# Optimization experiments

Measured on AMD Instinct MI355X. Metric: run time of the kernel, lower is better.

## Reference

```python
import jax, jax.numpy as jnp
import numpy as np

NUM_EMBEDDINGS = 8192
EMBED_DIM = 256
BETA = 0.25  # commitment loss weight (self.beta in the torch module)


def setup_inputs() -> dict:
    key = jax.random.key(0)
    k1, k2 = jax.random.split(key)
    z = jax.random.normal(k1, (16, EMBED_DIM, 32, 32), dtype=jnp.float32)
    # learned codebook (nn.Embedding weight), default init ~ N(0,1); scale for realism
    codebook = jax.random.normal(k2, (NUM_EMBEDDINGS, EMBED_DIM), dtype=jnp.float32)
    return {"z": z, "codebook": codebook}


def reference(z, codebook):
    # channel_last: [B, C, H, W] -> [B, H, W, C]
    zl = jnp.transpose(z, (0, 2, 3, 1))
    # d = ||e||^2 - 2 z.e  (the ||z||^2 term is constant w.r.t. argmin, as in source)
    d = jnp.sum(codebook * codebook, axis=1) - 2.0 * jnp.einsum('bhwd,nd->bhwn', zl, codebook)
    index = jnp.argmin(d, axis=-1)          # [B, H, W] int
    z_q = codebook[index]                   # [B, H, W, C]
    loss = (jnp.mean((jax.lax.stop_gradient(z_q) - zl) ** 2)
            + BETA * jnp.mean((z_q - jax.lax.stop_gradient(zl)) ** 2))
    # straight-through estimator
    z_q_st = zl + jax.lax.stop_gradient(z_q - zl)
    # diversity: mean over batch of (#unique codes used per sample) / (#positions per sample)
    B = index.shape[0]
    flat = index.reshape(B, -1)             # [B, HW]
    presence = jnp.zeros((B, NUM_EMBEDDINGS), jnp.float32).at[
        jnp.arange(B)[:, None], flat].set(1.0)
    diversity = presence.sum() / jnp.float32(flat.size)
    # channel_first: [B, H, W, C] -> [B, C, H, W]
    z_q_out = jnp.transpose(z_q_st, (0, 3, 1, 2))
    return z_q_out, index, loss, diversity
```

## Files before the change

### kernel.cpp

```cpp
#include <hip/hip_runtime.h>
#include <cstdint>

typedef unsigned short u16;
typedef unsigned int   u32;
typedef __attribute__((ext_vector_type(8))) short bf16x8;
typedef __attribute__((ext_vector_type(4))) float f32x4;

#define NPOS    16384
#define DIM     256
#define NCODES  8192
#define ZSTRIDE 262144
#define NELEM   4194304
#define TAU     6e-3f
#define RCH     32


#define WS_AHI    0u
#define WS_ALO    8388608u
#define WS_BHI    16777216u
#define WS_BLO    20971520u
#define WS_E2     25165824u
#define WS_WV1    25198592u
#define WS_WI1    25722880u
#define WS_WV2    26247168u
#define WS_IDX    26771456u
#define WS_PRES   26836992u
#define WS_RCNT   26853376u
#define WS_LDEL   26853380u
#define WS_RLIST  26853632u
#define WS_PART   26919168u
#define WS_RBV    26920448u
#define WS_RBI    29017600u

__device__ __forceinline__ u16 f2bf(float x) {
    u32 u = __float_as_uint(x);
    return (u16)((u + 0x7FFFu + ((u >> 16) & 1u)) >> 16);
}
__device__ __forceinline__ float bf2f(u16 h) { return __uint_as_float((u32)h << 16); }

__device__ __forceinline__ void gload_lds16(const void* g, void* l) {
    __builtin_amdgcn_global_load_lds(
        (const __attribute__((address_space(1))) void*)g,
        (__attribute__((address_space(3))) void*)l, 16, 0, 0);
}

__device__ __forceinline__ void top2_push(float& v1, int& i1, float& v2, float d, int c) {
    const bool better = d < v1;
    v2 = fminf(v2, fmaxf(d, v1));
    v1 = fminf(v1, d);
    if (better) i1 = c;
}
__device__ __forceinline__ void top2_merge(float& v1, int& i1, float& v2,
                                           float ov1, int oi1, float ov2) {
    const bool better = ov1 < v1;
    v2 = fminf(fminf(v2, ov2), fmaxf(v1, ov1));
    v1 = fminf(v1, ov1);
    if (better) i1 = oi1;
}

__global__ __launch_bounds__(256)
void preprocess(const float* __restrict__ cb, const float* __restrict__ z,
                u16* __restrict__ Bhi, u16* __restrict__ Blo,
                u16* __restrict__ Ahi, u16* __restrict__ Alo,
                float* __restrict__ e2, u32* __restrict__ presence,
                int* __restrict__ rcnt, float* __restrict__ ldel) {
    __shared__ u16 his[128 * 34], los[128 * 34];
    const int bid = blockIdx.x;
    const int t   = threadIdx.x;

    if (bid < 2048) {
        if (bid < 16) presence[bid * 256 + t] = 0u;
        if (bid == 16 && t == 0) { rcnt[0] = 0; ldel[0] = 0.0f; }

        const int row  = bid * 4 + (t >> 6);
        const int lane = t & 63;
        const float4 v = *(const float4*)(cb + (size_t)row * DIM + lane * 4);
        float s = v.x * v.x + v.y * v.y + v.z * v.z + v.w * v.w;
#pragma unroll
        for (int o = 32; o > 0; o >>= 1) s += __shfl_xor(s, o);
        if (lane == 0) e2[row] = s;

        const float vv[4] = {v.x, v.y, v.z, v.w};
        u16 h[4], l[4];
#pragma unroll
        for (int j = 0; j < 4; ++j) { h[j] = f2bf(vv[j]); l[j] = f2bf(vv[j] - bf2f(h[j])); }

        const int nt = row >> 7, pr = row & 127, kt = lane >> 3;
        const int q  = (lane & 7) >> 1, off = (lane & 1) * 4;
        const int sw = (pr >> 1) & 3;
        const size_t dst = ((size_t)(nt * 8 + kt) * 128 + pr) * 32 + ((q ^ sw) << 3) + off;
        *(uint2*)(Bhi + dst) = make_uint2((u32)h[0] | ((u32)h[1] << 16), (u32)h[2] | ((u32)h[3] << 16));
        *(uint2*)(Blo + dst) = make_uint2((u32)l[0] | ((u32)l[1] << 16), (u32)l[2] | ((u32)l[3] << 16));
        return;
    }

    const int zb = bid - 2048;
    const int m = zb >> 3, kt = zb & 7;
    const int b = m >> 3, hw0 = (m & 7) * 128;
    const int p = t & 127, ch = t >> 7;

#pragma unroll
    for (int sub = 0; sub < 16; ++sub) {
        const int cl = sub * 2 + ch;
        const float v = z[(size_t)b * ZSTRIDE + (size_t)(kt * 32 + cl) * 1024 + hw0 + p];
        const u16 h = f2bf(v);
        his[p * 34 + cl] = h;
        los[p * 34 + cl] = f2bf(v - bf2f(h));
    }
    __syncthreads();
    const int p2 = t >> 1, c0 = (t & 1) * 2;
    const int sw = (p2 >> 1) & 3;
    const size_t base = ((size_t)(m * 8 + kt) * 128 + p2) * 32;
    u32 wh[8], wl[8];
    const int half = c0 * 8;
#pragma unroll
    for (int j = 0; j < 8; ++j) {
        wh[j] = (u32)his[p2 * 34 + half + 2 * j] | ((u32)his[p2 * 34 + half + 2 * j + 1] << 16);
        wl[j] = (u32)los[p2 * 34 + half + 2 * j] | ((u32)los[p2 * 34 + half + 2 * j + 1] << 16);
    }
    *(uint4*)(Ahi + base + (((c0 + 0) ^ sw) << 3)) = make_uint4(wh[0], wh[1], wh[2], wh[3]);
    *(uint4*)(Ahi + base + (((c0 + 1) ^ sw) << 3)) = make_uint4(wh[4], wh[5], wh[6], wh[7]);
    *(uint4*)(Alo + base + (((c0 + 0) ^ sw) << 3)) = make_uint4(wl[0], wl[1], wl[2], wl[3]);
    *(uint4*)(Alo + base + (((c0 + 1) ^ sw) << 3)) = make_uint4(wl[4], wl[5], wl[6], wl[7]);
}

__global__ __launch_bounds__(256, 2)
void gemm_argmin(const u16* __restrict__ Ahi, const u16* __restrict__ Alo,
                 const u16* __restrict__ Bhi, const u16* __restrict__ Blo,
                 const float* __restrict__ e2,
                 float* __restrict__ wv1, int* __restrict__ wi1, float* __restrict__ wv2) {
    __shared__ u16 sbuf[2][4][4096];
    __shared__ float lv1[256]; __shared__ int li1[256]; __shared__ float lv2[256];

    const int bid = blockIdx.x;
    const int ng  = bid & 7;
    const int mt  = bid >> 3;

    const int tid  = threadIdx.x;
    const int lane = tid & 63;
    const int wvi  = tid >> 6;
    const int wr   = wvi >> 1, wc = wvi & 1;
    const int l15  = lane & 15, lq = lane >> 4;
    const int woff = (tid & 192) * 16;
    const int src  = tid * 8;
    const int sel  = (l15 >> 1) & 3;
    const int ka   = ((lq ^ sel) << 3);

#define FRAG(base, row) (*(const bf16x8*)((base) + (row) * 32 + ka))
#define STAGE(bq, ss_) do {                                                     \
        const int nt_ = ng * 8 + ((ss_) >> 3), kt_ = (ss_) & 7;                 \
        const u16* Ah_ = Ahi + (size_t)(mt * 8 + kt_) * 4096;                   \
        const u16* Al_ = Alo + (size_t)(mt * 8 + kt_) * 4096;                   \
        const u16* Bh_ = Bhi + (size_t)(nt_ * 8 + kt_) * 4096;                  \
        const u16* Bl_ = Blo + (size_t)(nt_ * 8 + kt_) * 4096;                  \
        gload_lds16(Ah_ + src,        (char*)&sbuf[bq][0][0] + woff);           \
        gload_lds16(Ah_ + 2048 + src, (char*)&sbuf[bq][0][0] + 4096 + woff);    \
        gload_lds16(Al_ + src,        (char*)&sbuf[bq][1][0] + woff);           \
        gload_lds16(Al_ + 2048 + src, (char*)&sbuf[bq][1][0] + 4096 + woff);    \
        gload_lds16(Bh_ + src,        (char*)&sbuf[bq][2][0] + woff);           \
        gload_lds16(Bh_ + 2048 + src, (char*)&sbuf[bq][2][0] + 4096 + woff);    \
        gload_lds16(Bl_ + src,        (char*)&sbuf[bq][3][0] + woff);           \
        gload_lds16(Bl_ + 2048 + src, (char*)&sbuf[bq][3][0] + 4096 + woff);    \
    } while (0)

    float rv1[16], rv2[16]; int ri1[16];
#pragma unroll
    for (int e = 0; e < 16; ++e) { rv1[e] = 3e38f; rv2[e] = 3e38f; ri1[e] = 0; }

    f32x4 acc[4][4] = {};
    float e2v[4];
    int cbase = 0;

    STAGE(0, 0);
    __syncthreads();

    for (int ss = 0; ss < 64; ++ss) {
        const int cur = ss & 1;
        if (ss < 63) STAGE(cur ^ 1, ss + 1);

        if ((ss & 7) == 0) {
            const int nt = ng * 8 + (ss >> 3);
            cbase = nt * 128 + wc * 64 + l15;
#pragma unroll
            for (int ni = 0; ni < 4; ++ni) e2v[ni] = e2[cbase + ni * 16];
        }

        const u16* Ah = &sbuf[cur][0][0];
        const u16* Al = &sbuf[cur][1][0];
        const u16* Bh = &sbuf[cur][2][0];
        const u16* Bl = &sbuf[cur][3][0];

        bf16x8 ah[4], bh[4], xx[4];
#pragma unroll
        for (int i = 0; i < 4; ++i) ah[i] = FRAG(Ah, wr * 64 + i * 16 + l15);
#pragma unroll
        for (int i = 0; i < 4; ++i) bh[i] = FRAG(Bh, wc * 64 + i * 16 + l15);
#pragma unroll
        for (int i = 0; i < 4; ++i)
#pragma unroll
            for (int j = 0; j < 4; ++j)
                acc[i][j] = __builtin_amdgcn_mfma_f32_16x16x32_bf16(ah[i], bh[j], acc[i][j], 0, 0, 0);
#pragma unroll
        for (int i = 0; i < 4; ++i) xx[i] = FRAG(Bl, wc * 64 + i * 16 + l15);
#pragma unroll
        for (int i = 0; i < 4; ++i)
#pragma unroll
            for (int j = 0; j < 4; ++j)
                acc[i][j] = __builtin_amdgcn_mfma_f32_16x16x32_bf16(ah[i], xx[j], acc[i][j], 0, 0, 0);
#pragma unroll
        for (int i = 0; i < 4; ++i) xx[i] = FRAG(Al, wr * 64 + i * 16 + l15);
#pragma unroll
        for (int i = 0; i < 4; ++i)
#pragma unroll
            for (int j = 0; j < 4; ++j)
                acc[i][j] = __builtin_amdgcn_mfma_f32_16x16x32_bf16(xx[i], bh[j], acc[i][j], 0, 0, 0);

        if ((ss & 7) == 7) {
#pragma unroll
            for (int mi = 0; mi < 4; ++mi)
#pragma unroll
                for (int j = 0; j < 4; ++j) {
                    const int e = mi * 4 + j;
#pragma unroll
                    for (int ni = 0; ni < 4; ++ni) {
                        const float d = fmaf(-2.0f, acc[mi][ni][j], e2v[ni]);
                        top2_push(rv1[e], ri1[e], rv2[e], d, cbase + ni * 16);
                    }
                }
#pragma unroll
            for (int mi = 0; mi < 4; ++mi)
#pragma unroll
                for (int ni = 0; ni < 4; ++ni)
                    acc[mi][ni] = f32x4{0.f, 0.f, 0.f, 0.f};
        }
        __syncthreads();
    }

#pragma unroll
    for (int mi = 0; mi < 4; ++mi)
#pragma unroll
        for (int j = 0; j < 4; ++j) {
            const int e = mi * 4 + j;
            float v1 = rv1[e], v2 = rv2[e]; int i1 = ri1[e];
#pragma unroll
            for (int off = 1; off <= 8; off <<= 1) {
                const float ov1 = __shfl_xor(v1, off);
                const int   oi1 = __shfl_xor(i1, off);
                const float ov2 = __shfl_xor(v2, off);
                top2_merge(v1, i1, v2, ov1, oi1, ov2);
            }
            if (l15 == 0) {
                const int row = wr * 64 + mi * 16 + lq * 4 + j;
                lv1[row * 2 + wc] = v1; li1[row * 2 + wc] = i1; lv2[row * 2 + wc] = v2;
            }
        }
    __syncthreads();
    if (tid < 128) {
        float v1 = lv1[tid * 2], v2 = lv2[tid * 2]; int i1 = li1[tid * 2];
        top2_merge(v1, i1, v2, lv1[tid * 2 + 1], li1[tid * 2 + 1], lv2[tid * 2 + 1]);
        const size_t o = (size_t)ng * NPOS + (size_t)mt * 128 + tid;
        wv1[o] = v1; wi1[o] = i1; wv2[o] = v2;
    }
#undef FRAG
#undef STAGE
}

__global__ __launch_bounds__(256)
void merge_output(const float* __restrict__ wv1, const int* __restrict__ wi1,
                  const float* __restrict__ wv2,
                  const float* __restrict__ z, const float* __restrict__ cb,
                  float* __restrict__ out, float* __restrict__ out_idxf,
                  float* __restrict__ partial, u32* __restrict__ presence,
                  int* __restrict__ rcnt, int* __restrict__ rlist,
                  int* __restrict__ ws_idx) {
    __shared__ int codes[64];
    __shared__ float red[256];
    const int tile = blockIdx.x;
    const int b    = tile >> 4;
    const int hw0  = (tile & 15) * 64;
    const int tid  = threadIdx.x;
    const int m    = tid & 63;
    const int cg   = tid >> 6;

    if (cg == 0) {
        const int pos = tile * 64 + m;
        float v1 = 3e38f, v2 = 3e38f; int i1 = 0;
#pragma unroll
        for (int g = 0; g < 8; ++g) {
            const size_t o = (size_t)g * NPOS + pos;
            top2_merge(v1, i1, v2, wv1[o], wi1[o], wv2[o]);
        }
        codes[m]      = i1;
        ws_idx[pos]   = i1;
        out_idxf[pos] = (float)i1;
        if (v2 - v1 < TAU) {
            const int s = atomicAdd(rcnt, 1);
            rlist[s] = pos;
        } else {
            atomicOr(&presence[b * 256 + (i1 >> 5)], 1u << (i1 & 31));
        }
    }
    __syncthreads();

    const int code = codes[m];
    const float* crow = cb  + (size_t)code * DIM;
    const float* zb   = z   + (size_t)b * ZSTRIDE + hw0 + m;
    float*       ob   = out + (size_t)b * ZSTRIDE + hw0 + m;

    float lsum = 0.0f;
#pragma unroll
    for (int q = 0; q < 16; ++q) {
        const int c = (cg * 16 + q) * 4;
        const float4 e = *(const float4*)(crow + c);
        const float z0 = zb[(size_t)(c + 0) * 1024];
        const float z1 = zb[(size_t)(c + 1) * 1024];
        const float z2 = zb[(size_t)(c + 2) * 1024];
        const float z3 = zb[(size_t)(c + 3) * 1024];
        const float d0 = e.x - z0, d1 = e.y - z1, d2 = e.z - z2, d3 = e.w - z3;
        lsum += d0 * d0 + d1 * d1 + d2 * d2 + d3 * d3;
        ob[(size_t)(c + 0) * 1024] = z0 + d0;
        ob[(size_t)(c + 1) * 1024] = z1 + d1;
        ob[(size_t)(c + 2) * 1024] = z2 + d2;
        ob[(size_t)(c + 3) * 1024] = z3 + d3;
    }
    red[tid] = lsum;
    __syncthreads();
    for (int o = 128; o > 0; o >>= 1) {
        if (tid < o) red[tid] += red[tid + o];
        __syncthreads();
    }
    if (tid == 0) partial[tile] = red[0];
}

__global__ __launch_bounds__(256)
void rescue_scan(const float* __restrict__ z, const float* __restrict__ cb,
                 const float* __restrict__ e2, const int* __restrict__ rcnt,
                 const int* __restrict__ rlist,
                 float* __restrict__ rbv, int* __restrict__ rbi) {
    __shared__ float zvec[256];
    __shared__ float sv[256]; __shared__ int si[256];
    const int n = rcnt[0];
    const int t = threadIdx.x;
    for (int idx = blockIdx.x; idx < n * RCH; idx += gridDim.x) {
        const int e  = idx >> 5;
        const int ch = idx & 31;
        const int pos = rlist[e];
        const int b = pos >> 10, hw = pos & 1023;
        __syncthreads();
        zvec[t] = z[(size_t)b * ZSTRIDE + (size_t)t * 1024 + hw];
        __syncthreads();

        const int c = ch * 256 + t;
        const float* cr = cb + (size_t)c * DIM;
        float a0 = 0.f, a1 = 0.f, a2 = 0.f, a3 = 0.f;
#pragma unroll
        for (int k = 0; k < DIM; k += 16) {
            const float4 v0 = *(const float4*)(cr + k);
            const float4 v1 = *(const float4*)(cr + k + 4);
            const float4 v2 = *(const float4*)(cr + k + 8);
            const float4 v3 = *(const float4*)(cr + k + 12);
            a0 = fmaf(zvec[k + 0], v0.x, a0); a0 = fmaf(zvec[k + 1], v0.y, a0);
            a0 = fmaf(zvec[k + 2], v0.z, a0); a0 = fmaf(zvec[k + 3], v0.w, a0);
            a1 = fmaf(zvec[k + 4], v1.x, a1); a1 = fmaf(zvec[k + 5], v1.y, a1);
            a1 = fmaf(zvec[k + 6], v1.z, a1); a1 = fmaf(zvec[k + 7], v1.w, a1);
            a2 = fmaf(zvec[k + 8], v2.x, a2); a2 = fmaf(zvec[k + 9], v2.y, a2);
            a2 = fmaf(zvec[k +10], v2.z, a2); a2 = fmaf(zvec[k +11], v2.w, a2);
            a3 = fmaf(zvec[k +12], v3.x, a3); a3 = fmaf(zvec[k +13], v3.y, a3);
            a3 = fmaf(zvec[k +14], v3.z, a3); a3 = fmaf(zvec[k +15], v3.w, a3);
        }
        const float dot = (a0 + a1) + (a2 + a3);
        sv[t] = fmaf(-2.f, dot, e2[c]); si[t] = c;
        __syncthreads();
        for (int o = 128; o > 0; o >>= 1) {
            if (t < o) {
                const float ov = sv[t + o]; const int oi = si[t + o];
                if (ov < sv[t] || (ov == sv[t] && oi < si[t])) { sv[t] = ov; si[t] = oi; }
            }
            __syncthreads();
        }
        if (t == 0) { rbv[e * RCH + ch] = sv[0]; rbi[e * RCH + ch] = si[0]; }
    }
}

__global__ __launch_bounds__(256)
void rescue_fix(const float* __restrict__ z, const float* __restrict__ cb,
                const int* __restrict__ rcnt, const int* __restrict__ rlist,
                const float* __restrict__ rbv, const int* __restrict__ rbi,
                const int* __restrict__ ws_idx,
                float* __restrict__ out_idxf, u32* __restrict__ presence,
                float* __restrict__ out, float* __restrict__ ldel) {
    __shared__ int   bestc;
    __shared__ float red[4];
    const int n = rcnt[0];
    const int t = threadIdx.x;
    for (int e = blockIdx.x; e < n; e += gridDim.x) {
        const int pos = rlist[e];
        const int b = pos >> 10, hw = pos & 1023;
        if (t == 0) {
            float bv = 3e38f; int bi = 0x7fffffff;
            for (int ch = 0; ch < RCH; ++ch) {
                const float v = rbv[e * RCH + ch]; const int i = rbi[e * RCH + ch];
                if (v < bv || (v == bv && i < bi)) { bv = v; bi = i; }
            }
            bestc = bi;
            out_idxf[pos] = (float)bi;
            atomicOr(&presence[b * 256 + (bi >> 5)], 1u << (bi & 31));
        }
        __syncthreads();
        const int best = bestc;
        const int old  = ws_idx[pos];
        if (best != old) {
            const float zv = z[(size_t)b * ZSTRIDE + (size_t)t * 1024 + hw];
            const float en = cb[(size_t)best * DIM + t];
            const float eo = cb[(size_t)old  * DIM + t];
            const float dn = en - zv, dold = eo - zv;
            out[(size_t)b * ZSTRIDE + (size_t)t * 1024 + hw] = zv + dn;
            float dl = dn * dn - dold * dold;
#pragma unroll
            for (int o = 32; o > 0; o >>= 1) dl += __shfl_xor(dl, o);
            if ((t & 63) == 0) red[t >> 6] = dl;
            __syncthreads();
            if (t == 0) atomicAdd(ldel, red[0] + red[1] + red[2] + red[3]);
        }
        __syncthreads();
    }
}

__global__ __launch_bounds__(256)
void finalize_kernel(const float* __restrict__ partial,
                     const u32* __restrict__ presence,
                     const float* __restrict__ ldel,
                     float* __restrict__ out_loss, float* __restrict__ out_div) {
    __shared__ float sred[256];
    __shared__ int   ired[256];
    const int tid = threadIdx.x;
    float s = partial[tid];
    int cnt = 0;
    for (int w = tid; w < 16 * 256; w += 256) cnt += __popc(presence[w]);
    sred[tid] = s; ired[tid] = cnt;
    __syncthreads();
    for (int o = 128; o > 0; o >>= 1) {
        if (tid < o) { sred[tid] += sred[tid + o]; ired[tid] += ired[tid + o]; }
        __syncthreads();
    }
    if (tid == 0) {
        out_loss[0] = 1.25f * (sred[0] + ldel[0]) / (float)NELEM;
        out_div[0]  = (float)ired[0] / (float)NPOS;
    }
}

extern "C" void kernel_launch(void* const* d_in, const int* in_sizes, int n_in,
                              void* d_out, int out_size, void* d_ws, size_t ws_size,
                              hipStream_t stream) {
    const float* z  = (const float*)d_in[0];
    const float* cb = (const float*)d_in[1];
    float* out = (float*)d_out;
    char*  ws  = (char*)d_ws;

    u16*   Ahi = (u16*)(ws + WS_AHI);
    u16*   Alo = (u16*)(ws + WS_ALO);
    u16*   Bhi = (u16*)(ws + WS_BHI);
    u16*   Blo = (u16*)(ws + WS_BLO);
    float* e2  = (float*)(ws + WS_E2);
    float* wv1 = (float*)(ws + WS_WV1);
    int*   wi1 = (int*)(ws + WS_WI1);
    float* wv2 = (float*)(ws + WS_WV2);
    int*   ws_idx = (int*)(ws + WS_IDX);
    u32*   presence = (u32*)(ws + WS_PRES);
    int*   rcnt  = (int*)(ws + WS_RCNT);
    float* ldel  = (float*)(ws + WS_LDEL);
    int*   rlist = (int*)(ws + WS_RLIST);
    float* partial = (float*)(ws + WS_PART);
    float* rbv = (float*)(ws + WS_RBV);
    int*   rbi = (int*)(ws + WS_RBI);

    float* out_zq   = out;
    float* out_idxf = out + NELEM;
    float* out_loss = out + NELEM + NPOS;
    float* out_div  = out + NELEM + NPOS + 1;

    preprocess<<<3072, 256, 0, stream>>>(cb, z, Bhi, Blo, Ahi, Alo, e2, presence, rcnt, ldel);
    gemm_argmin<<<1024, 256, 0, stream>>>(Ahi, Alo, Bhi, Blo, e2, wv1, wi1, wv2);
    merge_output<<<NPOS / 64, 256, 0, stream>>>(wv1, wi1, wv2, z, cb, out_zq, out_idxf,
                                                partial, presence, rcnt, rlist, ws_idx);
    rescue_scan<<<2048, 256, 0, stream>>>(z, cb, e2, rcnt, rlist, rbv, rbi);
    rescue_fix<<<256, 256, 0, stream>>>(z, cb, rcnt, rlist, rbv, rbi, ws_idx,
                                        out_idxf, presence, out_zq, ldel);
    finalize_kernel<<<1, 256, 0, stream>>>(partial, presence, ldel, out_loss, out_div);
}
```

Measured before the change: 256.5 us.

## Replace split-bf16 three-pass GEMM with single fp16 MFMA pass and wider rescue margin

```diff
diff --git a/kernel.cpp b/kernel.cpp
--- a/kernel.cpp
+++ b/kernel.cpp
@@ -3,7 +3,7 @@
 
 typedef unsigned short u16;
 typedef unsigned int   u32;
-typedef __attribute__((ext_vector_type(8))) short bf16x8;
+typedef __attribute__((ext_vector_type(8))) _Float16 f16x8;
 typedef __attribute__((ext_vector_type(4))) float f32x4;
 
 #define NPOS    16384
@@ -11,32 +11,29 @@
 #define NCODES  8192
 #define ZSTRIDE 262144
 #define NELEM   4194304
-#define TAU     6e-3f
+#define TAU     0.10f
 #define RCH     32
 
 
-#define WS_AHI    0u
-#define WS_ALO    8388608u
-#define WS_BHI    16777216u
-#define WS_BLO    20971520u
-#define WS_E2     25165824u
-#define WS_WV1    25198592u
-#define WS_WI1    25722880u
-#define WS_WV2    26247168u
-#define WS_IDX    26771456u
-#define WS_PRES   26836992u
-#define WS_RCNT   26853376u
-#define WS_LDEL   26853380u
-#define WS_RLIST  26853632u
-#define WS_PART   26919168u
-#define WS_RBV    26920448u
-#define WS_RBI    29017600u
-
-__device__ __forceinline__ u16 f2bf(float x) {
-    u32 u = __float_as_uint(x);
-    return (u16)((u + 0x7FFFu + ((u >> 16) & 1u)) >> 16);
-}
-__device__ __forceinline__ float bf2f(u16 h) { return __uint_as_float((u32)h << 16); }
+#define WS_A      0u
+#define WS_B      8388608u
+#define WS_E2     12582912u
+#define WS_WV1    12615680u
+#define WS_WI1    13139968u
+#define WS_WV2    13664256u
+#define WS_IDX    14188544u
+#define WS_PRES   14254080u
+#define WS_RCNT   14270464u
+#define WS_LDEL   14270468u
+#define WS_RLIST  14270720u
+#define WS_PART   14336256u
+#define WS_RBV    14337280u
+#define WS_RBI    16434432u
+
+__device__ __forceinline__ u16 f2h(float x) {
+    const _Float16 h = (_Float16)x;
+    return *(const u16*)&h;
+}
 
 __device__ __forceinline__ void gload_lds16(const void* g, void* l) {
     __builtin_amdgcn_global_load_lds(
@@ -60,11 +57,10 @@
 
 __global__ __launch_bounds__(256)
 void preprocess(const float* __restrict__ cb, const float* __restrict__ z,
-                u16* __restrict__ Bhi, u16* __restrict__ Blo,
-                u16* __restrict__ Ahi, u16* __restrict__ Alo,
+                u16* __restrict__ B, u16* __restrict__ A,
                 float* __restrict__ e2, u32* __restrict__ presence,
                 int* __restrict__ rcnt, float* __restrict__ ldel) {
-    __shared__ u16 his[128 * 34], los[128 * 34];
+    __shared__ u16 his[128 * 34];
     const int bid = blockIdx.x;
     const int t   = threadIdx.x;
 
@@ -80,17 +76,12 @@
         for (int o = 32; o > 0; o >>= 1) s += __shfl_xor(s, o);
         if (lane == 0) e2[row] = s;
 
-        const float vv[4] = {v.x, v.y, v.z, v.w};
-        u16 h[4], l[4];
-#pragma unroll
-        for (int j = 0; j < 4; ++j) { h[j] = f2bf(vv[j]); l[j] = f2bf(vv[j] - bf2f(h[j])); }
-
         const int nt = row >> 7, pr = row & 127, kt = lane >> 3;
         const int q  = (lane & 7) >> 1, off = (lane & 1) * 4;
         const int sw = (pr >> 1) & 3;
         const size_t dst = ((size_t)(nt * 8 + kt) * 128 + pr) * 32 + ((q ^ sw) << 3) + off;
-        *(uint2*)(Bhi + dst) = make_uint2((u32)h[0] | ((u32)h[1] << 16), (u32)h[2] | ((u32)h[3] << 16));
-        *(uint2*)(Blo + dst) = make_uint2((u32)l[0] | ((u32)l[1] << 16), (u32)l[2] | ((u32)l[3] << 16));
+        *(uint2*)(B + dst) = make_uint2((u32)f2h(v.x) | ((u32)f2h(v.y) << 16),
+                                        (u32)f2h(v.z) | ((u32)f2h(v.w) << 16));
         return;
     }
 
@@ -103,33 +94,26 @@
     for (int sub = 0; sub < 16; ++sub) {
         const int cl = sub * 2 + ch;
         const float v = z[(size_t)b * ZSTRIDE + (size_t)(kt * 32 + cl) * 1024 + hw0 + p];
-        const u16 h = f2bf(v);
-        his[p * 34 + cl] = h;
-        los[p * 34 + cl] = f2bf(v - bf2f(h));
+        his[p * 34 + cl] = f2h(v);
     }
     __syncthreads();
     const int p2 = t >> 1, c0 = (t & 1) * 2;
     const int sw = (p2 >> 1) & 3;
     const size_t base = ((size_t)(m * 8 + kt) * 128 + p2) * 32;
-    u32 wh[8], wl[8];
+    u32 wh[8];
     const int half = c0 * 8;
 #pragma unroll
-    for (int j = 0; j < 8; ++j) {
+    for (int j = 0; j < 8; ++j)
         wh[j] = (u32)his[p2 * 34 + half + 2 * j] | ((u32)his[p2 * 34 + half + 2 * j + 1] << 16);
-        wl[j] = (u32)los[p2 * 34 + half + 2 * j] | ((u32)los[p2 * 34 + half + 2 * j + 1] << 16);
-    }
-    *(uint4*)(Ahi + base + (((c0 + 0) ^ sw) << 3)) = make_uint4(wh[0], wh[1], wh[2], wh[3]);
-    *(uint4*)(Ahi + base + (((c0 + 1) ^ sw) << 3)) = make_uint4(wh[4], wh[5], wh[6], wh[7]);
-    *(uint4*)(Alo + base + (((c0 + 0) ^ sw) << 3)) = make_uint4(wl[0], wl[1], wl[2], wl[3]);
-    *(uint4*)(Alo + base + (((c0 + 1) ^ sw) << 3)) = make_uint4(wl[4], wl[5], wl[6], wl[7]);
+    *(uint4*)(A + base + (((c0 + 0) ^ sw) << 3)) = make_uint4(wh[0], wh[1], wh[2], wh[3]);
+    *(uint4*)(A + base + (((c0 + 1) ^ sw) << 3)) = make_uint4(wh[4], wh[5], wh[6], wh[7]);
 }
 
 __global__ __launch_bounds__(256, 2)
-void gemm_argmin(const u16* __restrict__ Ahi, const u16* __restrict__ Alo,
-                 const u16* __restrict__ Bhi, const u16* __restrict__ Blo,
+void gemm_argmin(const u16* __restrict__ A, const u16* __restrict__ B,
                  const float* __restrict__ e2,
                  float* __restrict__ wv1, int* __restrict__ wi1, float* __restrict__ wv2) {
-    __shared__ u16 sbuf[2][4][4096];
+    __shared__ u16 sbuf[2][2][4096];
     __shared__ float lv1[256]; __shared__ int li1[256]; __shared__ float lv2[256];
 
     const int bid = blockIdx.x;
@@ -146,21 +130,15 @@
     const int sel  = (l15 >> 1) & 3;
     const int ka   = ((lq ^ sel) << 3);
 
-#define FRAG(base, row) (*(const bf16x8*)((base) + (row) * 32 + ka))
+#define FRAG(base, row) (*(const f16x8*)((base) + (row) * 32 + ka))
 #define STAGE(bq, ss_) do {                                                     \
         const int nt_ = ng * 8 + ((ss_) >> 3), kt_ = (ss_) & 7;                 \
-        const u16* Ah_ = Ahi + (size_t)(mt * 8 + kt_) * 4096;                   \
-        const u16* Al_ = Alo + (size_t)(mt * 8 + kt_) * 4096;                   \
-        const u16* Bh_ = Bhi + (size_t)(nt_ * 8 + kt_) * 4096;                  \
-        const u16* Bl_ = Blo + (size_t)(nt_ * 8 + kt_) * 4096;                  \
-        gload_lds16(Ah_ + src,        (char*)&sbuf[bq][0][0] + woff);           \
-        gload_lds16(Ah_ + 2048 + src, (char*)&sbuf[bq][0][0] + 4096 + woff);    \
-        gload_lds16(Al_ + src,        (char*)&sbuf[bq][1][0] + woff);           \
-        gload_lds16(Al_ + 2048 + src, (char*)&sbuf[bq][1][0] + 4096 + woff);    \
-        gload_lds16(Bh_ + src,        (char*)&sbuf[bq][2][0] + woff);           \
-        gload_lds16(Bh_ + 2048 + src, (char*)&sbuf[bq][2][0] + 4096 + woff);    \
-        gload_lds16(Bl_ + src,        (char*)&sbuf[bq][3][0] + woff);           \
-        gload_lds16(Bl_ + 2048 + src, (char*)&sbuf[bq][3][0] + 4096 + woff);    \
+        const u16* Ap_ = A + (size_t)(mt * 8 + kt_) * 4096;                     \
+        const u16* Bp_ = B + (size_t)(nt_ * 8 + kt_) * 4096;                    \
+        gload_lds16(Ap_ + src,        (char*)&sbuf[bq][0][0] + woff);           \
+        gload_lds16(Ap_ + 2048 + src, (char*)&sbuf[bq][0][0] + 4096 + woff);    \
+        gload_lds16(Bp_ + src,        (char*)&sbuf[bq][1][0] + woff);           \
+        gload_lds16(Bp_ + 2048 + src, (char*)&sbuf[bq][1][0] + 4096 + woff);    \
     } while (0)
 
     float rv1[16], rv2[16]; int ri1[16];
@@ -185,35 +163,19 @@
             for (int ni = 0; ni < 4; ++ni) e2v[ni] = e2[cbase + ni * 16];
         }
 
-        const u16* Ah = &sbuf[cur][0][0];
-        const u16* Al = &sbuf[cur][1][0];
-        const u16* Bh = &sbuf[cur][2][0];
-        const u16* Bl = &sbuf[cur][3][0];
-
-        bf16x8 ah[4], bh[4], xx[4];
-#pragma unroll
-        for (int i = 0; i < 4; ++i) ah[i] = FRAG(Ah, wr * 64 + i * 16 + l15);
-#pragma unroll
-        for (int i = 0; i < 4; ++i) bh[i] = FRAG(Bh, wc * 64 + i * 16 + l15);
+        const u16* Ap = &sbuf[cur][0][0];
+        const u16* Bp = &sbuf[cur][1][0];
+
+        f16x8 af[4], bf[4];
+#pragma unroll
+        for (int i = 0; i < 4; ++i) af[i] = FRAG(Ap, wr * 64 + i * 16 + l15);
+#pragma unroll
+        for (int i = 0; i < 4; ++i) bf[i] = FRAG(Bp, wc * 64 + i * 16 + l15);
 #pragma unroll
         for (int i = 0; i < 4; ++i)
 #pragma unroll
             for (int j = 0; j < 4; ++j)
-                acc[i][j] = __builtin_amdgcn_mfma_f32_16x16x32_bf16(ah[i], bh[j], acc[i][j], 0, 0, 0);
-#pragma unroll
-        for (int i = 0; i < 4; ++i) xx[i] = FRAG(Bl, wc * 64 + i * 16 + l15);
-#pragma unroll
-        for (int i = 0; i < 4; ++i)
-#pragma unroll
-            for (int j = 0; j < 4; ++j)
-                acc[i][j] = __builtin_amdgcn_mfma_f32_16x16x32_bf16(ah[i], xx[j], acc[i][j], 0, 0, 0);
-#pragma unroll
-        for (int i = 0; i < 4; ++i) xx[i] = FRAG(Al, wr * 64 + i * 16 + l15);
-#pragma unroll
-        for (int i = 0; i < 4; ++i)
-#pragma unroll
-            for (int j = 0; j < 4; ++j)
-                acc[i][j] = __builtin_amdgcn_mfma_f32_16x16x32_bf16(xx[i], bh[j], acc[i][j], 0, 0, 0);
+                acc[i][j] = __builtin_amdgcn_mfma_f32_16x16x32_f16(af[i], bf[j], acc[i][j], 0, 0, 0);
 
         if ((ss & 7) == 7) {
 #pragma unroll
@@ -457,10 +419,8 @@
     float* out = (float*)d_out;
     char*  ws  = (char*)d_ws;
 
-    u16*   Ahi = (u16*)(ws + WS_AHI);
-    u16*   Alo = (u16*)(ws + WS_ALO);
-    u16*   Bhi = (u16*)(ws + WS_BHI);
-    u16*   Blo = (u16*)(ws + WS_BLO);
+    u16*   A   = (u16*)(ws + WS_A);
+    u16*   B   = (u16*)(ws + WS_B);
     float* e2  = (float*)(ws + WS_E2);
     float* wv1 = (float*)(ws + WS_WV1);
     int*   wi1 = (int*)(ws + WS_WI1);
@@ -479,8 +439,8 @@
     float* out_loss = out + NELEM + NPOS;
     float* out_div  = out + NELEM + NPOS + 1;
 
-    preprocess<<<3072, 256, 0, stream>>>(cb, z, Bhi, Blo, Ahi, Alo, e2, presence, rcnt, ldel);
-    gemm_argmin<<<1024, 256, 0, stream>>>(Ahi, Alo, Bhi, Blo, e2, wv1, wi1, wv2);
+    preprocess<<<3072, 256, 0, stream>>>(cb, z, B, A, e2, presence, rcnt, ldel);
+    gemm_argmin<<<1024, 256, 0, stream>>>(A, B, e2, wv1, wi1, wv2);
     merge_output<<<NPOS / 64, 256, 0, stream>>>(wv1, wi1, wv2, z, cb, out_zq, out_idxf,
                                                 partial, presence, rcnt, rlist, ws_idx);
     rescue_scan<<<2048, 256, 0, stream>>>(z, cb, e2, rcnt, rlist, rbv, rbi);
```

New measurement: 338.6 us. +32.0%, slower.
